# Kernel optimization log

Measured on AMD Instinct MI355X. Metric: run time of the kernel, lower is better.

## Reference

```python
import jax, jax.numpy as jnp
import numpy as np

B, S, D, H, W1, G = 2, 4096, 768, 12, 256, 8  # W1 = one-sided window (attention_window // 2)
HD = D // H
NC = S // W1  # number of query chunks of size W1
NEG = -1e9


def setup_inputs():
    key = jax.random.key(0)
    ks = jax.random.split(key, 9)
    def w(k):
        return jax.random.normal(k, (D, D), jnp.float32) * 0.02
    zb = jnp.zeros((D,), jnp.float32)
    # mask: >0 global, 0 local, <0 masked. First G tokens are global.
    mask = jnp.zeros((B, 1, 1, S), jnp.int32).at[:, :, :, :G].set(1)
    return {
        "hidden_states": jax.random.normal(ks[0], (B, S, D), jnp.float32),
        "attention_mask": mask,
        "Wq": w(ks[1]), "bq": zb,
        "Wk": w(ks[2]), "bk": zb,
        "Wv": w(ks[3]), "bv": zb,
        "Wqg": w(ks[4]), "bqg": zb,
        "Wkg": w(ks[5]), "bkg": zb,
        "Wvg": w(ks[6]), "bvg": zb,
        "Wo": w(ks[7]), "bo": zb,
        "n_global": G,
    }


def reference(hidden_states, attention_mask, Wq, bq, Wk, bk, Wv, bv,
              Wqg, bqg, Wkg, bkg, Wvg, bvg, Wo, bo, n_global):
    g = n_global
    mask = attention_mask.reshape(B, S)
    key_neg = mask < 0  # masked-out positions
    scale = 1.0 / np.sqrt(HD)

    def heads(x):  # [B,S,D] -> [B,H,S,HD]
        return x.reshape(B, S, H, HD).transpose(0, 2, 1, 3)

    q = heads(hidden_states @ Wq + bq) * scale
    k = heads(hidden_states @ Wk + bk)
    v = heads(hidden_states @ Wv + bv)

    # ---- sliding-window (banded) scores via 3-chunk gather ----
    idx = jnp.arange(NC)[:, None] * W1 + jnp.arange(3 * W1)[None, :]  # [NC,3W] into padded seq
    k_ch = jnp.pad(k, ((0, 0), (0, 0), (W1, W1), (0, 0)))[:, :, idx]  # [B,H,NC,3W,HD]
    q_ch = q.reshape(B, H, NC, W1, HD)
    band = jnp.einsum('bhcqd,bhckd->bhcqk', q_ch, k_ch)  # [B,H,NC,W,3W]

    qi = jnp.arange(W1)
    kj = jnp.arange(3 * W1)
    band_ok = jnp.abs(kj[None, :] - W1 - qi[:, None]) <= W1        # [W,3W] |j-i|<=w
    j_abs = idx - W1                                               # absolute key index
    in_range = (j_abs >= 0) & (j_abs < S)                          # [NC,3W]
    neg_ch = jnp.pad(key_neg, ((0, 0), (W1, W1)))[:, idx]          # [B,NC,3W]
    valid = (band_ok[None, None, None]
             & in_range[None, None, :, None, :]
             & (~neg_ch)[:, None, :, None, :])                     # [B,1,NC,W,3W]
    band = jnp.where(valid, band, NEG)

    # ---- scores of every query against the global keys (regular k proj) ----
    glob = jnp.einsum('bhsd,bhgd->bhsg', q, k[:, :, :g])           # [B,H,S,G]
    glob = jnp.where(key_neg[:, None, None, :g], NEG, glob)

    scores = jnp.concatenate([glob.reshape(B, H, NC, W1, g), band], axis=-1)
    probs = jax.nn.softmax(scores, axis=-1)
    probs = jnp.where(key_neg.reshape(B, 1, NC, W1, 1), 0.0, probs)  # zero masked query rows

    v_ch = jnp.pad(v, ((0, 0), (0, 0), (W1, W1), (0, 0)))[:, :, idx]
    out = jnp.einsum('bhcqk,bhckd->bhcqd', probs[..., g:], v_ch)
    out = out + jnp.einsum('bhcqg,bhgd->bhcqd', probs[..., :g], v[:, :, :g])
    out = out.reshape(B, H, S, HD)

    # ---- global tokens: full attention with dedicated global projections ----
    qg = heads(hidden_states @ Wqg + bqg)[:, :, :g] * scale        # [B,H,G,HD]
    kg = heads(hidden_states @ Wkg + bkg)
    vg = heads(hidden_states @ Wvg + bvg)
    gs = jnp.einsum('bhgd,bhsd->bhgs', qg, kg)                     # [B,H,G,S]
    gs = jnp.where(key_neg[:, None, None, :], NEG, gs)
    gp = jax.nn.softmax(gs, axis=-1)
    og = jnp.einsum('bhgs,bhsd->bhgd', gp, vg)
    out = out.at[:, :, :g].set(og)

    merged = out.transpose(0, 2, 1, 3).reshape(B, S, D)
    return merged @ Wo + bo  # outer output projection
```

## Files before the change

### kernel.cpp

```cpp
#include <hip/hip_runtime.h>

#define BB 2
#define SS 4096
#define DD 768
#define HH 12
#define HDD 64
#define W1C 256
#define NCC 16
#define GG 8

typedef unsigned short u16;
typedef __attribute__((ext_vector_type(4))) unsigned short u16x4;
typedef __attribute__((ext_vector_type(8))) unsigned short u16x8;
typedef __attribute__((ext_vector_type(8))) short s16x8;
typedef __attribute__((ext_vector_type(4))) float f32x4;

__device__ __forceinline__ float b2f(u16 u) {
  union { unsigned int i; float f; } v;
  v.i = ((unsigned int)u) << 16;
  return v.f;
}
__device__ __forceinline__ u16 f2b(float f) {
  union { float f; unsigned int i; } v;
  v.f = f;
  unsigned int r = v.i + 0x7FFFu + ((v.i >> 16) & 1u);
  return (u16)(r >> 16);
}
__device__ __forceinline__ float fexp2(float x) {
#if __has_builtin(__builtin_amdgcn_exp2f)
  return __builtin_amdgcn_exp2f(x);
#else
  return exp2f(x);
#endif
}
__device__ __forceinline__ unsigned pk_bf16(float lo, float hi) {
  unsigned r;
  asm("v_cvt_pk_bf16_f32 %0, %1, %2" : "=v"(r) : "v"(lo), "v"(hi));
  return r;
}
__device__ __forceinline__ void load_lds16(const void* g, void* l) {
  __builtin_amdgcn_global_load_lds(
      (const __attribute__((address_space(1))) unsigned int*)g,
      (__attribute__((address_space(3))) unsigned int*)l, 16, 0, 0);
}

#define QSCALE 0.18033688011112042f

__global__ __launch_bounds__(256) void cvt_f32_bf16(
    const float* __restrict__ in, u16* __restrict__ out, int n8) {
  int i = blockIdx.x * 256 + threadIdx.x;
  if (i >= n8) return;
  const float4* p = (const float4*)(in + (size_t)i * 8);
  float4 a = p[0], b = p[1];
  u16x8 o;
  o[0] = f2b(a.x); o[1] = f2b(a.y); o[2] = f2b(a.z); o[3] = f2b(a.w);
  o[4] = f2b(b.x); o[5] = f2b(b.y); o[6] = f2b(b.z); o[7] = f2b(b.w);
  *(u16x8*)(out + (size_t)i * 8) = o;
}

struct WtArgs { const float* W[6]; };

__global__ __launch_bounds__(256) void transpose_wt(WtArgs wa,
                                                    u16* __restrict__ WT) {
  __shared__ float T[64][65];
  const int mat = blockIdx.z;
  const int k0 = blockIdx.y * 64;
  const int n0 = blockIdx.x * 64;
  const float* __restrict__ W = wa.W[mat];
  const int t = threadIdx.x;
#pragma unroll
  for (int i = 0; i < 4; i++) {
    int idx4 = t + i * 256;
    int r = idx4 >> 4, c4 = idx4 & 15;
    float4 v = *(const float4*)(W + (size_t)(k0 + r) * 768 + n0 + c4 * 4);
    T[r][c4 * 4 + 0] = v.x; T[r][c4 * 4 + 1] = v.y;
    T[r][c4 * 4 + 2] = v.z; T[r][c4 * 4 + 3] = v.w;
  }
  __syncthreads();
#pragma unroll
  for (int i = 0; i < 2; i++) {
    int ci = t + i * 256;
    int nl = ci >> 3, k8 = ci & 7;
    u16x8 o;
#pragma unroll
    for (int jj = 0; jj < 8; jj++) o[jj] = f2b(T[k8 * 8 + jj][nl]);
    *(u16x8*)(WT + ((size_t)mat * 768 + n0 + nl) * 768 + k0 + k8 * 8) = o;
  }
}

struct BiasArgs { const float* bias[5]; };

template <int MODE>
__global__ __launch_bounds__(512, 1) void gemm_bf16(
    const u16* __restrict__ A, const u16* __restrict__ WT, BiasArgs ba,
    u16* __restrict__ outb, float* __restrict__ outf) {
  constexpr int NTL = (MODE == 0) ? 15 : 3;
  constexpr int NWG = 64 * NTL;
  constexpr int NT = 12;
  constexpr int ABYTES = 128 * 64 * 2;
  constexpr int BBYTES = 256 * 64 * 2;
  constexpr int BUFB = ABYTES + BBYTES;

  extern __shared__ __align__(16) char smem[];

  const int tid = threadIdx.x;
  const int w = tid >> 6, l = tid & 63;
  const int lq = l & 15, g = l >> 4;
  const int wm = w >> 2, wn = w & 3;

  const int cpx = NWG >> 3;
  const int id = (int)blockIdx.x;
  const int swz = (id & 7) * cpx + (id >> 3);
  const int bm = swz / NTL, bn = swz % NTL;
  const int m0 = bm * 128;
  const int nw0 = bn * 256;
  const int wsel = (MODE == 0) ? (bn / 3) : 0;
  const int nmat0 = (MODE == 0) ? ((bn % 3) * 256) : (bn * 256);
  const float* __restrict__ bias = ba.bias[wsel];

  f32x4 acc[4][4];
#pragma unroll
  for (int i = 0; i < 4; i++)
#pragma unroll
    for (int j = 0; j < 4; j++) acc[i][j] = (f32x4){0.f, 0.f, 0.f, 0.f};

  auto stage = [&](int t) {
    const int k0 = t * 64;
    char* uA = smem + (t % 3) * BUFB;
    char* uB = uA + ABYTES;
#pragma unroll
    for (int j = 0; j < 2; j++) {
      const int ci = j * 8 + w;
      const int p = ci * 64 + l;
      const int row = p >> 3, sl = p & 7;
      load_lds16(A + (size_t)(m0 + row) * 768 + k0 + ((sl ^ (row & 7)) * 8),
                 uA + ci * 1024);
    }
#pragma unroll
    for (int j = 0; j < 4; j++) {
      const int ci = j * 8 + w;
      const int p = ci * 64 + l;
      const int row = p >> 3, sl = p & 7;
      load_lds16(WT + (size_t)(nw0 + row) * 768 + k0 + ((sl ^ (row & 7)) * 8),
                 uB + ci * 1024);
    }
  };

  stage(0);
  stage(1);
  asm volatile("s_waitcnt vmcnt(6)" ::: "memory");
  __builtin_amdgcn_sched_barrier(0);
  __builtin_amdgcn_s_barrier();
  __builtin_amdgcn_sched_barrier(0);

  for (int kt = 0; kt < NT; kt++) {
    const u16* rA = (const u16*)(smem + (kt % 3) * BUFB);
    const u16* rB = (const u16*)(smem + (kt % 3) * BUFB + ABYTES);

    if (kt < NT - 2) stage(kt + 2);
    __builtin_amdgcn_sched_barrier(0);

    s16x8 af[4][2], bf[4][2];
#pragma unroll
    for (int mi = 0; mi < 4; mi++) {
      const int r = wm * 64 + mi * 16 + lq;
#pragma unroll
      for (int ks = 0; ks < 2; ks++)
        af[mi][ks] =
            *(const s16x8*)(rA + r * 64 + (((ks * 4 + g) ^ (r & 7)) * 8));
    }
#pragma unroll
    for (int nj = 0; nj < 4; nj++) {
      const int r = wn * 64 + nj * 16 + lq;
#pragma unroll
      for (int ks = 0; ks < 2; ks++)
        bf[nj][ks] =
            *(const s16x8*)(rB + r * 64 + (((ks * 4 + g) ^ (r & 7)) * 8));
    }
#pragma unroll
    for (int mi = 0; mi < 4; mi++)
#pragma unroll
      for (int nj = 0; nj < 4; nj++)
#pragma unroll
        for (int ks = 0; ks < 2; ks++)
          acc[mi][nj] = __builtin_amdgcn_mfma_f32_16x16x32_bf16(
              af[mi][ks], bf[nj][ks], acc[mi][nj], 0, 0, 0);

    if (kt < NT - 2)
      asm volatile("s_waitcnt vmcnt(6)" ::: "memory");
    else
      asm volatile("s_waitcnt vmcnt(0)" ::: "memory");
    __builtin_amdgcn_sched_barrier(0);
    __builtin_amdgcn_s_barrier();
    __builtin_amdgcn_sched_barrier(0);
  }

  if (MODE == 0) {
    const float scale = (wsel == 0) ? QSCALE : 1.0f;
    u16* outw = outb + (size_t)wsel * ((size_t)BB * HH * SS * HDD);
#pragma unroll
    for (int nj = 0; nj < 4; nj++) {
      const int c = nmat0 + wn * 64 + nj * 16 + lq;
      const float bv = bias[c];
      const int h = c >> 6, hd = c & 63;
#pragma unroll
      for (int mi = 0; mi < 4; mi++) {
#pragma unroll
        for (int r = 0; r < 4; r++) {
          const int m = m0 + wm * 64 + mi * 16 + g * 4 + r;
          const int b = m >> 12, s = m & 4095;
          outw[((size_t)(b * HH + h) * SS + s) * HDD + hd] =
              f2b((acc[mi][nj][r] + bv) * scale);
        }
      }
    }
  } else {
#pragma unroll
    for (int nj = 0; nj < 4; nj++) {
      const int c = nmat0 + wn * 64 + nj * 16 + lq;
      const float bv = bias[c];
#pragma unroll
      for (int mi = 0; mi < 4; mi++) {
#pragma unroll
        for (int r = 0; r < 4; r++) {
          const int m = m0 + wm * 64 + mi * 16 + g * 4 + r;
          outf[(size_t)m * 768 + c] = acc[mi][nj][r] + bv;
        }
      }
    }
  }
}

__global__ __launch_bounds__(256) void qg_proj(
    const float* __restrict__ hs, const float* __restrict__ Wqg,
    const float* __restrict__ bqg, u16* __restrict__ QG) {
  __shared__ float hsL[8][768];
  const int bh = blockIdx.x;
  const int b = bh / HH, h = bh % HH;
  const int t = threadIdx.x;
#pragma unroll
  for (int i = 0; i < 6; i++) {
    int idx = t + i * 256;
    int row = idx / 192, c4 = idx % 192;
    *(float4*)&hsL[row][c4 * 4] =
        *(const float4*)(hs + ((size_t)b * SS + row) * DD + c4 * 4);
  }
  __syncthreads();
#pragma unroll
  for (int rep = 0; rep < 2; rep++) {
    int qi = rep * 4 + (t >> 6);
    int d = t & 63, n = h * 64 + d;
    float acc = bqg[n];
    for (int k = 0; k < DD; k++)
      acc = fmaf(hsL[qi][k], Wqg[(size_t)k * DD + n], acc);
    QG[((size_t)bh * 16 + qi) * 64 + d] = f2b(acc * QSCALE);
  }
#pragma unroll
  for (int i = 0; i < 2; i++) {
    int idx = t + i * 256;
    int row = 8 + (idx >> 6), d = idx & 63;
    QG[((size_t)bh * 16 + row) * 64 + d] = 0;
  }
}

template <int GLOBAL>
__global__ __launch_bounds__(256) void attn_mfma(
    const u16* __restrict__ Q, const u16* __restrict__ K,
    const u16* __restrict__ V, const int* __restrict__ amask,
    u16* __restrict__ ATT, float* __restrict__ Pnum,
    float* __restrict__ Pden) {
  extern __shared__ __align__(16) char smem[];
  const int tid = threadIdx.x;
  const int w = tid >> 6, lane = tid & 63;
  const int lq = lane & 15, g = lane >> 4;
  const int h = blockIdx.y, b = blockIdx.z;
  const int bh = b * HH + h;
  const size_t bhs = (size_t)bh * SS;
  const int q0 = GLOBAL ? 0 : (int)blockIdx.x * 64;
  const int split = GLOBAL ? (int)blockIdx.x : 0;

  char* Kl;
  char* VT;
  if constexpr (GLOBAL) {
    Kl = smem + w * 16384;
    VT = Kl + 8192;
  } else {
    Kl = smem;
    VT = smem + 8192;
  }

  s16x8 qf[2];
  {
    const u16* qp = GLOBAL ? (Q + ((size_t)bh * 16 + lq) * 64)
                           : (Q + (bhs + q0 + w * 16 + lq) * 64);
    qf[0] = *(const s16x8*)(qp + g * 8);
    qf[1] = *(const s16x8*)(qp + 32 + g * 8);
  }

  f32x4 oacc[4];
#pragma unroll
  for (int i = 0; i < 4; i++) oacc[i] = (f32x4){0.f, 0.f, 0.f, 0.f};
  float denom = 0.f;

  const int NT = GLOBAL ? 2 : 10;
  for (int kt = 0; kt < NT; kt++) {
    int j0, klimit;
    bool bandfree;
    if constexpr (GLOBAL) {
      j0 = split * 512 + (w * 2 + kt) * 64;
      bandfree = true;
      klimit = 64;
    } else {
      if (kt < 9) { j0 = q0 - 256 + kt * 64; bandfree = false; klimit = 64; }
      else        { j0 = 0;                  bandfree = true;  klimit = 8; }
    }

    int jm = j0 + lane;
    int mv = ((unsigned)jm < (unsigned)SS) ? amask[b * SS + jm] : -1;
    bool okk = (mv >= 0) && (lane < klimit);
    unsigned long long vm = __ballot(okk);

    if constexpr (GLOBAL) {
      asm volatile("s_waitcnt lgkmcnt(0)" ::: "memory");
      const u16* Ks = K + bhs * 64 + (size_t)j0 * 64;
#pragma unroll
      for (int i = 0; i < 8; i++) {
        int ci = i * 64 + lane;
        int row = ci >> 3, cc = ci & 7, cs = cc ^ (row & 7);
        load_lds16(Ks + row * 64 + cs * 8, Kl + i * 1024);
      }
      const u16* Vs = V + bhs * 64 + (size_t)j0 * 64;
#pragma unroll
      for (int p = 0; p < 8; p++) {
        u16x8 vv = *(const u16x8*)(Vs + (size_t)lane * 64 + p * 8);
#pragma unroll
        for (int e = 0; e < 8; e++)
          *(u16*)(VT + (p * 8 + e) * 128 + ((lane * 2) ^ (e << 4))) = vv[e];
      }
      asm volatile("s_waitcnt vmcnt(0) lgkmcnt(0)" ::: "memory");
    } else {
      __syncthreads();
      if (j0 >= 0 && j0 + 64 <= SS) {
        const u16* Ks = K + bhs * 64 + (size_t)j0 * 64;
#pragma unroll
        for (int i = 0; i < 2; i++) {
          int ci = (i * 4 + w) * 64 + lane;
          int row = ci >> 3, cc = ci & 7, cs = cc ^ (row & 7);
          load_lds16(Ks + row * 64 + cs * 8, Kl + (i * 4 + w) * 1024);
        }
      } else {
#pragma unroll
        for (int i = 0; i < 2; i++) {
          int ci = (i * 4 + w) * 64 + lane;
          int row = ci >> 3, cc = ci & 7, cs = cc ^ (row & 7);
          int jj = j0 + row;
          u16x8 val;
#pragma unroll
          for (int e = 0; e < 8; e++) val[e] = 0;
          if ((unsigned)jj < (unsigned)SS)
            val = *(const u16x8*)(K + (bhs + jj) * 64 + cs * 8);
          *(u16x8*)(Kl + ci * 16) = val;
        }
      }
#pragma unroll
      for (int p = 0; p < 2; p++) {
        int d0 = p * 32 + w * 8;
        int jj = j0 + lane;
        u16x8 vv;
#pragma unroll
        for (int e = 0; e < 8; e++) vv[e] = 0;
        if ((unsigned)jj < (unsigned)SS)
          vv = *(const u16x8*)(V + (bhs + jj) * 64 + d0);
#pragma unroll
        for (int e = 0; e < 8; e++)
          *(u16*)(VT + (d0 + e) * 128 + ((lane * 2) ^ (e << 4))) = vv[e];
      }
      asm volatile("s_waitcnt vmcnt(0)" ::: "memory");
      __syncthreads();
    }

    f32x4 sc[4];
#pragma unroll
    for (int i = 0; i < 4; i++) sc[i] = (f32x4){0.f, 0.f, 0.f, 0.f};
#pragma unroll
    for (int s = 0; s < 2; s++) {
#pragma unroll
      for (int ks = 0; ks < 4; ks++) {
        s16x8 kf = *(const s16x8*)(Kl + (ks * 16 + lq) * 128 +
                                   (((s * 4 + g) ^ (lq & 7)) << 4));
        sc[ks] = __builtin_amdgcn_mfma_f32_16x16x32_bf16(kf, qf[s], sc[ks],
                                                          0, 0, 0);
      }
    }

    {
      const unsigned mlo = (unsigned)vm, mhi = (unsigned)(vm >> 32);
      const int q_abs = q0 + w * 16 + lq;
      bool allin = bandfree;
      if constexpr (!GLOBAL) {
        const int qw = q0 + w * 16;
        allin = bandfree || (j0 >= qw - 241 && j0 <= qw + 193);
      }
      const bool fast = (vm == ~0ull) && allin;
      const int ddq = j0 + g * 4 - q_abs;
      const int gsh = g * 4;
      if (fast) {
#pragma unroll
        for (int ks = 0; ks < 4; ks++)
#pragma unroll
          for (int r = 0; r < 4; r++) {
            float p = fexp2(sc[ks][r]);
            sc[ks][r] = p;
            denom += p;
          }
      } else {
#pragma unroll
        for (int ks = 0; ks < 4; ks++)
#pragma unroll
          for (int r = 0; r < 4; r++) {
            float e = fexp2(sc[ks][r]);
            unsigned bit =
                ((ks < 2 ? mlo : mhi) >> (gsh + ((ks & 1) * 16 + r))) & 1u;
            bool ok = bit && (allin ||
                              (unsigned)(ddq + ks * 16 + r + 256) <= 512u);
            float p = ok ? e : 0.f;
            sc[ks][r] = p;
            denom += p;
          }
      }
    }

#pragma unroll
    for (int s = 0; s < 2; s++) {
      const int srcA = lq + ((g & 1) << 5);
      const bool hiSel = g >= 2;
      float L[4], H[4];
#pragma unroll
      for (int r = 0; r < 4; r++) {
        float a0 = __shfl(sc[2 * s][r], srcA);
        float a1 = __shfl(sc[2 * s + 1][r], srcA);
        L[r] = hiSel ? a1 : a0;
        float b0 = __shfl(sc[2 * s][r], srcA + 16);
        float b1 = __shfl(sc[2 * s + 1][r], srcA + 16);
        H[r] = hiSel ? b1 : b0;
      }
      union { unsigned u[4]; s16x8 v; } pf;
      pf.u[0] = pk_bf16(L[0], L[1]);
      pf.u[1] = pk_bf16(L[2], L[3]);
      pf.u[2] = pk_bf16(H[0], H[1]);
      pf.u[3] = pk_bf16(H[2], H[3]);
#pragma unroll
      for (int dblk = 0; dblk < 4; dblk++) {
        s16x8 vf = *(const s16x8*)(VT + (dblk * 16 + lq) * 128 +
                                   (((s * 4 + g) ^ (lq & 7)) << 4));
        oacc[dblk] = __builtin_amdgcn_mfma_f32_16x16x32_bf16(vf, pf.v,
                                                              oacc[dblk],
                                                              0, 0, 0);
      }
    }
  }

  denom += __shfl_xor(denom, 16);
  denom += __shfl_xor(denom, 32);
  if constexpr (!GLOBAL) {
    const int q_abs = q0 + w * 16 + lq;
    const float rowscale = (amask[b * SS + q_abs] >= 0) ? (1.f / denom) : 0.f;
    u16* orow = ATT + ((size_t)b * SS + q_abs) * DD + h * 64;
#pragma unroll
    for (int dblk = 0; dblk < 4; dblk++) {
      u16x4 o;
#pragma unroll
      for (int r = 0; r < 4; r++) o[r] = f2b(oacc[dblk][r] * rowscale);
      *(u16x4*)(orow + dblk * 16 + g * 4) = o;
    }
  } else {
    const int pidx = split * 4 + w;
    float* np = Pnum + ((size_t)bh * 32 + pidx) * 1024;
#pragma unroll
    for (int dblk = 0; dblk < 4; dblk++)
#pragma unroll
      for (int r = 0; r < 4; r++)
        np[(dblk * 16 + g * 4 + r) * 16 + lq] = oacc[dblk][r];
    Pden[((size_t)bh * 32 + pidx) * 16 + lq] = denom;
  }
}

__global__ __launch_bounds__(512) void gmerge(const float* __restrict__ Pnum,
                                              const float* __restrict__ Pden,
                                              u16* __restrict__ ATT) {
  const int bh = blockIdx.x;
  const int b = bh / HH, h = bh % HH;
  const int t = threadIdx.x;
  const int q = t >> 6, d = t & 63;
  float num = 0.f, den = 0.f;
#pragma unroll 4
  for (int p = 0; p < 32; p++) {
    num += Pnum[((size_t)bh * 32 + p) * 1024 + d * 16 + q];
    den += Pden[((size_t)bh * 32 + p) * 16 + q];
  }
  ATT[((size_t)b * SS + q) * DD + h * 64 + d] = f2b(num / den);
}

extern "C" void kernel_launch(void* const* d_in, const int* in_sizes, int n_in,
                              void* d_out, int out_size, void* d_ws,
                              size_t ws_size, hipStream_t stream) {
  const float* hs = (const float*)d_in[0];
  const int* amask = (const int*)d_in[1];
  const float* Wq = (const float*)d_in[2];
  const float* bq = (const float*)d_in[3];
  const float* Wk = (const float*)d_in[4];
  const float* bk = (const float*)d_in[5];
  const float* Wv = (const float*)d_in[6];
  const float* bv = (const float*)d_in[7];
  const float* Wqg = (const float*)d_in[8];
  const float* bqg = (const float*)d_in[9];
  const float* Wkg = (const float*)d_in[10];
  const float* bkg = (const float*)d_in[11];
  const float* Wvg = (const float*)d_in[12];
  const float* bvg = (const float*)d_in[13];
  const float* Wo = (const float*)d_in[14];
  const float* bo = (const float*)d_in[15];
  float* out = (float*)d_out;

  char* ws = (char*)d_ws;
  const size_t QSZB = (size_t)BB * HH * SS * HDD * 2;
  u16* Qb = (u16*)(ws + 0);
  u16* Kb = (u16*)(ws + QSZB);
  u16* Vb = (u16*)(ws + 2 * QSZB);
  u16* KGb = (u16*)(ws + 3 * QSZB);
  u16* VGb = (u16*)(ws + 4 * QSZB);
  u16* Ab = (u16*)(ws + 5 * QSZB);
  u16* WTb = (u16*)(ws + 6 * QSZB);
  u16* ATTb = (u16*)(ws + 6 * QSZB + 7077888);
  u16* QGb = (u16*)(ws + 7 * QSZB + 7077888);
  float* Pnum = (float*)(ws + 7 * QSZB + 7077888 + 49152);
  float* Pden = (float*)(ws + 7 * QSZB + 7077888 + 49152 + 3145728);

  hipLaunchKernelGGL(cvt_f32_bf16, dim3(3072), dim3(256), 0, stream, hs, Ab,
                     (int)((size_t)BB * SS * DD / 8));

  WtArgs wa;
  wa.W[0] = Wq; wa.W[1] = Wk; wa.W[2] = Wv;
  wa.W[3] = Wkg; wa.W[4] = Wvg; wa.W[5] = Wo;
  hipLaunchKernelGGL(transpose_wt, dim3(12, 12, 6), dim3(256), 0, stream, wa,
                     WTb);

  BiasArgs b0;
  b0.bias[0] = bq; b0.bias[1] = bk; b0.bias[2] = bv;
  b0.bias[3] = bkg; b0.bias[4] = bvg;
  hipLaunchKernelGGL((gemm_bf16<0>), dim3(960), dim3(512), 147456, stream,
                     Ab, WTb, b0, Qb, (float*)nullptr);

  hipLaunchKernelGGL(qg_proj, dim3(24), dim3(256), 0, stream, hs, Wqg, bqg,
                     QGb);

  hipLaunchKernelGGL((attn_mfma<1>), dim3(8, HH, BB), dim3(256), 65536,
                     stream, QGb, KGb, VGb, amask, (u16*)nullptr, Pnum, Pden);

  hipLaunchKernelGGL((attn_mfma<0>), dim3(64, HH, BB), dim3(256), 16384,
                     stream, Qb, Kb, Vb, amask, ATTb, (float*)nullptr,
                     (float*)nullptr);

  hipLaunchKernelGGL(gmerge, dim3(24), dim3(512), 0, stream, Pnum, Pden, ATTb);

  BiasArgs b1;
  for (int i = 0; i < 5; i++) b1.bias[i] = bo;
  hipLaunchKernelGGL((gemm_bf16<1>), dim3(192), dim3(512), 147456, stream,
                     ATTb, WTb + (size_t)5 * 768 * 768, b1, (u16*)nullptr,
                     out);
}
```

Baseline: 203.1 us.

## Merge prep kernels into one launch and retile projection GEMM to BM256/BK32

Merges the f32-to-bf16 conversion, the weight transpose and the global-query projection into a single prep kernel to cut kernel launches. The projection GEMM moves to a 256-row M tile with a K step of 32, and A-fragment loads are split into two halves that alternate with MFMA groups under s_setprio. LDS drops from 147456 to 98304 bytes and the output GEMM uses a smaller buffer. The larger tile halves the workgroup count (480 over 256 CUs), which risks uneven load across CUs. The extra barrier per k-step adds synchronisation cost.

Measured after the change: 207.4 us. +2.1%, slower.

```diff
diff --git a/kernel.cpp b/kernel.cpp
--- a/kernel.cpp
+++ b/kernel.cpp
@@ -46,45 +46,77 @@
 
 #define QSCALE 0.18033688011112042f
 
-__global__ __launch_bounds__(256) void cvt_f32_bf16(
-    const float* __restrict__ in, u16* __restrict__ out, int n8) {
-  int i = blockIdx.x * 256 + threadIdx.x;
-  if (i >= n8) return;
-  const float4* p = (const float4*)(in + (size_t)i * 8);
-  float4 a = p[0], b = p[1];
-  u16x8 o;
-  o[0] = f2b(a.x); o[1] = f2b(a.y); o[2] = f2b(a.z); o[3] = f2b(a.w);
-  o[4] = f2b(b.x); o[5] = f2b(b.y); o[6] = f2b(b.z); o[7] = f2b(b.w);
-  *(u16x8*)(out + (size_t)i * 8) = o;
-}
-
 struct WtArgs { const float* W[6]; };
 
-__global__ __launch_bounds__(256) void transpose_wt(WtArgs wa,
-                                                    u16* __restrict__ WT) {
-  __shared__ float T[64][65];
-  const int mat = blockIdx.z;
-  const int k0 = blockIdx.y * 64;
-  const int n0 = blockIdx.x * 64;
-  const float* __restrict__ W = wa.W[mat];
+__global__ __launch_bounds__(256) void prep(
+    const float* __restrict__ hs, WtArgs wa, const float* __restrict__ Wqg,
+    const float* __restrict__ bqg, u16* __restrict__ Ab,
+    u16* __restrict__ WT, u16* __restrict__ QG) {
+  __shared__ __align__(16) char pshm[24576];
+  const int bid = blockIdx.x;
   const int t = threadIdx.x;
-#pragma unroll
-  for (int i = 0; i < 4; i++) {
-    int idx4 = t + i * 256;
-    int r = idx4 >> 4, c4 = idx4 & 15;
-    float4 v = *(const float4*)(W + (size_t)(k0 + r) * 768 + n0 + c4 * 4);
-    T[r][c4 * 4 + 0] = v.x; T[r][c4 * 4 + 1] = v.y;
-    T[r][c4 * 4 + 2] = v.z; T[r][c4 * 4 + 3] = v.w;
-  }
-  __syncthreads();
-#pragma unroll
-  for (int i = 0; i < 2; i++) {
-    int ci = t + i * 256;
-    int nl = ci >> 3, k8 = ci & 7;
+
+  if (bid < 3072) {
+    int i = bid * 256 + t;
+    const float4* p = (const float4*)(hs + (size_t)i * 8);
+    float4 a = p[0], b = p[1];
     u16x8 o;
-#pragma unroll
-    for (int jj = 0; jj < 8; jj++) o[jj] = f2b(T[k8 * 8 + jj][nl]);
-    *(u16x8*)(WT + ((size_t)mat * 768 + n0 + nl) * 768 + k0 + k8 * 8) = o;
+    o[0] = f2b(a.x); o[1] = f2b(a.y); o[2] = f2b(a.z); o[3] = f2b(a.w);
+    o[4] = f2b(b.x); o[5] = f2b(b.y); o[6] = f2b(b.z); o[7] = f2b(b.w);
+    *(u16x8*)(Ab + (size_t)i * 8) = o;
+  } else if (bid < 3936) {
+    float (*T)[65] = (float (*)[65])pshm;
+    const int t2 = bid - 3072;
+    const int mat = t2 / 144;
+    const int rem = t2 % 144;
+    const int k0 = (rem / 12) * 64;
+    const int n0 = (rem % 12) * 64;
+    const float* __restrict__ W = wa.W[mat];
+#pragma unroll
+    for (int i = 0; i < 4; i++) {
+      int idx4 = t + i * 256;
+      int r = idx4 >> 4, c4 = idx4 & 15;
+      float4 v = *(const float4*)(W + (size_t)(k0 + r) * 768 + n0 + c4 * 4);
+      T[r][c4 * 4 + 0] = v.x; T[r][c4 * 4 + 1] = v.y;
+      T[r][c4 * 4 + 2] = v.z; T[r][c4 * 4 + 3] = v.w;
+    }
+    __syncthreads();
+#pragma unroll
+    for (int i = 0; i < 2; i++) {
+      int ci = t + i * 256;
+      int nl = ci >> 3, k8 = ci & 7;
+      u16x8 o;
+#pragma unroll
+      for (int jj = 0; jj < 8; jj++) o[jj] = f2b(T[k8 * 8 + jj][nl]);
+      *(u16x8*)(WT + ((size_t)mat * 768 + n0 + nl) * 768 + k0 + k8 * 8) = o;
+    }
+  } else {
+    float (*hsL)[768] = (float (*)[768])pshm;
+    const int bh = bid - 3936;
+    const int b = bh / HH, h = bh % HH;
+#pragma unroll
+    for (int i = 0; i < 6; i++) {
+      int idx = t + i * 256;
+      int row = idx / 192, c4 = idx % 192;
+      *(float4*)&hsL[row][c4 * 4] =
+          *(const float4*)(hs + ((size_t)b * SS + row) * DD + c4 * 4);
+    }
+    __syncthreads();
+#pragma unroll
+    for (int rep = 0; rep < 2; rep++) {
+      int qi = rep * 4 + (t >> 6);
+      int d = t & 63, n = h * 64 + d;
+      float acc = bqg[n];
+      for (int k = 0; k < DD; k++)
+        acc = fmaf(hsL[qi][k], Wqg[(size_t)k * DD + n], acc);
+      QG[((size_t)bh * 16 + qi) * 64 + d] = f2b(acc * QSCALE);
+    }
+#pragma unroll
+    for (int i = 0; i < 2; i++) {
+      int idx = t + i * 256;
+      int row = 8 + (idx >> 6), d = idx & 63;
+      QG[((size_t)bh * 16 + row) * 64 + d] = 0;
+    }
   }
 }
 
@@ -94,12 +126,16 @@
 __global__ __launch_bounds__(512, 1) void gemm_bf16(
     const u16* __restrict__ A, const u16* __restrict__ WT, BiasArgs ba,
     u16* __restrict__ outb, float* __restrict__ outf) {
+  constexpr int BM = (MODE == 0) ? 256 : 128;
+  constexpr int WM = BM / 2;
+  constexpr int MR = BM / 32;
   constexpr int NTL = (MODE == 0) ? 15 : 3;
-  constexpr int NWG = 64 * NTL;
-  constexpr int NT = 12;
-  constexpr int ABYTES = 128 * 64 * 2;
-  constexpr int BBYTES = 256 * 64 * 2;
+  constexpr int NWG = (8192 / BM) * NTL;
+  constexpr int NT = 24;
+  constexpr int ABYTES = BM * 64;
+  constexpr int BBYTES = 256 * 64;
   constexpr int BUFB = ABYTES + BBYTES;
+  constexpr int ALD = BM / 128;
 
   extern __shared__ __align__(16) char smem[];
 
@@ -112,43 +148,44 @@
   const int id = (int)blockIdx.x;
   const int swz = (id & 7) * cpx + (id >> 3);
   const int bm = swz / NTL, bn = swz % NTL;
-  const int m0 = bm * 128;
+  const int m0 = bm * BM;
   const int nw0 = bn * 256;
   const int wsel = (MODE == 0) ? (bn / 3) : 0;
   const int nmat0 = (MODE == 0) ? ((bn % 3) * 256) : (bn * 256);
   const float* __restrict__ bias = ba.bias[wsel];
 
-  f32x4 acc[4][4];
-#pragma unroll
-  for (int i = 0; i < 4; i++)
+  f32x4 acc[MR][4];
+#pragma unroll
+  for (int i = 0; i < MR; i++)
 #pragma unroll
     for (int j = 0; j < 4; j++) acc[i][j] = (f32x4){0.f, 0.f, 0.f, 0.f};
 
   auto stage = [&](int t) {
-    const int k0 = t * 64;
+    const int k0 = t * 32;
     char* uA = smem + (t % 3) * BUFB;
     char* uB = uA + ABYTES;
 #pragma unroll
+    for (int j = 0; j < ALD; j++) {
+      const int p = j * 512 + tid;
+      const int row = p >> 2, sl = p & 3;
+      load_lds16(A + (size_t)(m0 + row) * 768 + k0 + ((sl ^ (row & 3)) * 8),
+                 uA + (j * 8 + w) * 1024);
+    }
+#pragma unroll
     for (int j = 0; j < 2; j++) {
-      const int ci = j * 8 + w;
-      const int p = ci * 64 + l;
-      const int row = p >> 3, sl = p & 7;
-      load_lds16(A + (size_t)(m0 + row) * 768 + k0 + ((sl ^ (row & 7)) * 8),
-                 uA + ci * 1024);
-    }
-#pragma unroll
-    for (int j = 0; j < 4; j++) {
-      const int ci = j * 8 + w;
-      const int p = ci * 64 + l;
-      const int row = p >> 3, sl = p & 7;
-      load_lds16(WT + (size_t)(nw0 + row) * 768 + k0 + ((sl ^ (row & 7)) * 8),
-                 uB + ci * 1024);
+      const int p = j * 512 + tid;
+      const int row = p >> 2, sl = p & 3;
+      load_lds16(WT + (size_t)(nw0 + row) * 768 + k0 + ((sl ^ (row & 3)) * 8),
+                 uB + (j * 8 + w) * 1024);
     }
   };
 
   stage(0);
   stage(1);
-  asm volatile("s_waitcnt vmcnt(6)" ::: "memory");
+  if constexpr (MODE == 0)
+    asm volatile("s_waitcnt vmcnt(4)" ::: "memory");
+  else
+    asm volatile("s_waitcnt vmcnt(3)" ::: "memory");
   __builtin_amdgcn_sched_barrier(0);
   __builtin_amdgcn_s_barrier();
   __builtin_amdgcn_sched_barrier(0);
@@ -160,36 +197,53 @@
     if (kt < NT - 2) stage(kt + 2);
     __builtin_amdgcn_sched_barrier(0);
 
-    s16x8 af[4][2], bf[4][2];
-#pragma unroll
-    for (int mi = 0; mi < 4; mi++) {
-      const int r = wm * 64 + mi * 16 + lq;
-#pragma unroll
-      for (int ks = 0; ks < 2; ks++)
-        af[mi][ks] =
-            *(const s16x8*)(rA + r * 64 + (((ks * 4 + g) ^ (r & 7)) * 8));
-    }
-#pragma unroll
-    for (int nj = 0; nj < 4; nj++) {
-      const int r = wn * 64 + nj * 16 + lq;
-#pragma unroll
-      for (int ks = 0; ks < 2; ks++)
-        bf[nj][ks] =
-            *(const s16x8*)(rB + r * 64 + (((ks * 4 + g) ^ (r & 7)) * 8));
-    }
+    const int so = (g ^ (lq & 3)) * 8;
+
+    s16x8 bf[4], af0[4];
+#pragma unroll
+    for (int nj = 0; nj < 4; nj++)
+      bf[nj] = *(const s16x8*)(rB + (wn * 64 + nj * 16 + lq) * 32 + so);
 #pragma unroll
     for (int mi = 0; mi < 4; mi++)
+      af0[mi] = *(const s16x8*)(rA + (wm * WM + mi * 16 + lq) * 32 + so);
+    __builtin_amdgcn_s_barrier();
+    asm volatile("s_waitcnt lgkmcnt(0)" ::: "memory");
+    __builtin_amdgcn_sched_barrier(0);
+    __builtin_amdgcn_s_setprio(1);
+#pragma unroll
+    for (int mi = 0; mi < 4; mi++)
 #pragma unroll
       for (int nj = 0; nj < 4; nj++)
-#pragma unroll
-        for (int ks = 0; ks < 2; ks++)
-          acc[mi][nj] = __builtin_amdgcn_mfma_f32_16x16x32_bf16(
-              af[mi][ks], bf[nj][ks], acc[mi][nj], 0, 0, 0);
-
-    if (kt < NT - 2)
-      asm volatile("s_waitcnt vmcnt(6)" ::: "memory");
-    else
+        acc[mi][nj] = __builtin_amdgcn_mfma_f32_16x16x32_bf16(
+            af0[mi], bf[nj], acc[mi][nj], 0, 0, 0);
+    __builtin_amdgcn_s_setprio(0);
+
+    if constexpr (MODE == 0) {
+      s16x8 af1[4];
+#pragma unroll
+      for (int mi = 0; mi < 4; mi++)
+        af1[mi] =
+            *(const s16x8*)(rA + (wm * WM + (mi + 4) * 16 + lq) * 32 + so);
+      asm volatile("s_waitcnt lgkmcnt(0)" ::: "memory");
+      __builtin_amdgcn_sched_barrier(0);
+      __builtin_amdgcn_s_setprio(1);
+#pragma unroll
+      for (int mi = 0; mi < 4; mi++)
+#pragma unroll
+        for (int nj = 0; nj < 4; nj++)
+          acc[mi + 4][nj] = __builtin_amdgcn_mfma_f32_16x16x32_bf16(
+              af1[mi], bf[nj], acc[mi + 4][nj], 0, 0, 0);
+      __builtin_amdgcn_s_setprio(0);
+    }
+
+    if (kt < NT - 2) {
+      if constexpr (MODE == 0)
+        asm volatile("s_waitcnt vmcnt(4)" ::: "memory");
+      else
+        asm volatile("s_waitcnt vmcnt(3)" ::: "memory");
+    } else {
       asm volatile("s_waitcnt vmcnt(0)" ::: "memory");
+    }
     __builtin_amdgcn_sched_barrier(0);
     __builtin_amdgcn_s_barrier();
     __builtin_amdgcn_sched_barrier(0);
@@ -204,10 +258,10 @@
       const float bv = bias[c];
       const int h = c >> 6, hd = c & 63;
 #pragma unroll
-      for (int mi = 0; mi < 4; mi++) {
+      for (int mi = 0; mi < MR; mi++) {
 #pragma unroll
         for (int r = 0; r < 4; r++) {
-          const int m = m0 + wm * 64 + mi * 16 + g * 4 + r;
+          const int m = m0 + wm * WM + mi * 16 + g * 4 + r;
           const int b = m >> 12, s = m & 4095;
           outw[((size_t)(b * HH + h) * SS + s) * HDD + hd] =
               f2b((acc[mi][nj][r] + bv) * scale);
@@ -220,46 +274,14 @@
       const int c = nmat0 + wn * 64 + nj * 16 + lq;
       const float bv = bias[c];
 #pragma unroll
-      for (int mi = 0; mi < 4; mi++) {
+      for (int mi = 0; mi < MR; mi++) {
 #pragma unroll
         for (int r = 0; r < 4; r++) {
-          const int m = m0 + wm * 64 + mi * 16 + g * 4 + r;
+          const int m = m0 + wm * WM + mi * 16 + g * 4 + r;
           outf[(size_t)m * 768 + c] = acc[mi][nj][r] + bv;
         }
       }
     }
-  }
-}
-
-__global__ __launch_bounds__(256) void qg_proj(
-    const float* __restrict__ hs, const float* __restrict__ Wqg,
-    const float* __restrict__ bqg, u16* __restrict__ QG) {
-  __shared__ float hsL[8][768];
-  const int bh = blockIdx.x;
-  const int b = bh / HH, h = bh % HH;
-  const int t = threadIdx.x;
-#pragma unroll
-  for (int i = 0; i < 6; i++) {
-    int idx = t + i * 256;
-    int row = idx / 192, c4 = idx % 192;
-    *(float4*)&hsL[row][c4 * 4] =
-        *(const float4*)(hs + ((size_t)b * SS + row) * DD + c4 * 4);
-  }
-  __syncthreads();
-#pragma unroll
-  for (int rep = 0; rep < 2; rep++) {
-    int qi = rep * 4 + (t >> 6);
-    int d = t & 63, n = h * 64 + d;
-    float acc = bqg[n];
-    for (int k = 0; k < DD; k++)
-      acc = fmaf(hsL[qi][k], Wqg[(size_t)k * DD + n], acc);
-    QG[((size_t)bh * 16 + qi) * 64 + d] = f2b(acc * QSCALE);
-  }
-#pragma unroll
-  for (int i = 0; i < 2; i++) {
-    int idx = t + i * 256;
-    int row = 8 + (idx >> 6), d = idx & 63;
-    QG[((size_t)bh * 16 + row) * 64 + d] = 0;
   }
 }
 
@@ -536,23 +558,17 @@
   float* Pnum = (float*)(ws + 7 * QSZB + 7077888 + 49152);
   float* Pden = (float*)(ws + 7 * QSZB + 7077888 + 49152 + 3145728);
 
-  hipLaunchKernelGGL(cvt_f32_bf16, dim3(3072), dim3(256), 0, stream, hs, Ab,
-                     (int)((size_t)BB * SS * DD / 8));
-
   WtArgs wa;
   wa.W[0] = Wq; wa.W[1] = Wk; wa.W[2] = Wv;
   wa.W[3] = Wkg; wa.W[4] = Wvg; wa.W[5] = Wo;
-  hipLaunchKernelGGL(transpose_wt, dim3(12, 12, 6), dim3(256), 0, stream, wa,
-                     WTb);
+  hipLaunchKernelGGL(prep, dim3(3960), dim3(256), 0, stream, hs, wa, Wqg,
+                     bqg, Ab, WTb, QGb);
 
   BiasArgs b0;
   b0.bias[0] = bq; b0.bias[1] = bk; b0.bias[2] = bv;
   b0.bias[3] = bkg; b0.bias[4] = bvg;
-  hipLaunchKernelGGL((gemm_bf16<0>), dim3(960), dim3(512), 147456, stream,
+  hipLaunchKernelGGL((gemm_bf16<0>), dim3(480), dim3(512), 98304, stream,
                      Ab, WTb, b0, Qb, (float*)nullptr);
-
-  hipLaunchKernelGGL(qg_proj, dim3(24), dim3(256), 0, stream, hs, Wqg, bqg,
-                     QGb);
 
   hipLaunchKernelGGL((attn_mfma<1>), dim3(8, HH, BB), dim3(256), 65536,
                      stream, QGb, KGb, VGb, amask, (u16*)nullptr, Pnum, Pden);
@@ -563,9 +579,8 @@
 
   hipLaunchKernelGGL(gmerge, dim3(24), dim3(512), 0, stream, Pnum, Pden, ATTb);
 
-  BiasArgs b1;
-  for (int i = 0; i < 5; i++) b1.bias[i] = bo;
-  hipLaunchKernelGGL((gemm_bf16<1>), dim3(192), dim3(512), 147456, stream,
-                     ATTb, WTb + (size_t)5 * 768 * 768, b1, (u16*)nullptr,
-                     out);
-}
+  hipLaunchKernelGGL((gemm_bf16<1>), dim3(192), dim3(512), 73728, stream,
+                     ATTb, WTb + (size_t)5 * 768 * 768,
+                     [&]{ BiasArgs b1; for (int i = 0; i < 5; i++) b1.bias[i] = bo; return b1; }(),
+                     (u16*)nullptr, out);
+}
```
